# Kernel optimization log

Measured on AMD Instinct MI355X. Metric: run time of the kernel, lower is better.

The kernel has to match this reference:

```python
import jax, jax.numpy as jnp
import numpy as np

E = 1024   # embed_dim
H = 8      # att_heads
HD = E // H
L = 4      # layer_num
B = 64
M = 256
EPS = 1e-5


def celu(x, alpha=1.3):
    return jnp.where(x > 0, x, alpha * jnp.expm1(x / alpha))


def group_norm(x, w, b):
    # x: [N, E], groups = H (GroupNorm over channel groups, per-sample)
    xg = x.reshape(-1, H, HD)
    mu = xg.mean(-1, keepdims=True)
    var = ((xg - mu) ** 2).mean(-1, keepdims=True)
    xg = (xg - mu) * jax.lax.rsqrt(var + EPS)
    return xg.reshape(-1, E) * w + b


def layer_norm(x, w, b):
    mu = x.mean(-1, keepdims=True)
    var = ((x - mu) ** 2).mean(-1, keepdims=True)
    return (x - mu) * jax.lax.rsqrt(var + EPS) * w + b


def setup_inputs() -> dict:
    key = jax.random.key(0)
    ks = jax.random.split(key, 20)
    s = 0.02
    return {
        "gv_feat": jnp.zeros((B, 1), jnp.float32),
        "att_feats": jax.random.normal(ks[0], (B, M, E), jnp.float32),
        "att_mask": jnp.ones((B, M), jnp.float32),
        "mem_W": jax.random.normal(ks[1], (L, E, E), jnp.float32) * s,
        "mem_b": jnp.zeros((L, E), jnp.float32),
        "gn_w": jnp.ones((L, E), jnp.float32),
        "gn_b": jnp.zeros((L, E), jnp.float32),
        "upd_W": jax.random.normal(ks[2], (L, 2 * HD, HD), jnp.float32) * s,
        "upd_b": jnp.zeros((L, HD), jnp.float32),
        "gate_W": jax.random.normal(ks[3], (L, 2 * HD, HD), jnp.float32) * s,
        "gate_b": jnp.zeros((L, HD), jnp.float32),
        "ln_w": jnp.ones((L, E), jnp.float32),
        "ln_b": jnp.zeros((L, E), jnp.float32),
        "proj_W": jax.random.normal(ks[4], ((L + 1) * E, E), jnp.float32) * s,
        "proj_b": jnp.zeros((E,), jnp.float32),
        "lnf_w": jnp.ones((E,), jnp.float32),
        "lnf_b": jnp.zeros((E,), jnp.float32),
    }


def reference(gv_feat, att_feats, att_mask, mem_W, mem_b, gn_w, gn_b,
              upd_W, upd_b, gate_W, gate_b, ln_w, ln_b,
              proj_W, proj_b, lnf_w, lnf_b):
    scaling = HD ** (-0.5)
    mask3 = att_mask[:, :, None]                       # [B, M, 1]
    msum = mask3.sum(1)                                # [B, 1]

    def pool(x):
        return (x * mask3).sum(1) / msum               # [B, E]

    # gv_feat has last dim 1 -> computed by masked mean pooling
    gv = pool(att_feats)
    feat_arr = [gv]
    x = att_feats
    key_mask = att_mask[:, None, None, :]              # [B, 1, 1, M]
    for i in range(L):
        mem = celu(x.reshape(-1, E) @ mem_W[i] + mem_b[i])
        mem = group_norm(mem, gn_w[i], gn_b[i])
        xh = x.reshape(B, M, H, HD).swapaxes(1, 2)     # [B, H, M, HD]
        mh = mem.reshape(B, M, H, HD).swapaxes(1, 2)   # [B, H, M, HD]
        attn = jnp.einsum('bhqd,bhkd->bhqk', xh, mh) * scaling
        attn = jnp.where(key_mask == 0, -1e9, attn)
        p = jax.nn.softmax(attn, axis=-1)
        ctx = jnp.einsum('bhqk,bhkd->bhqd', p, xh)     # values == xh
        inp = jnp.concatenate([xh, ctx], axis=-1)      # [B, H, M, 2*HD]
        f_t = jnp.tanh(jax.nn.relu(inp @ upd_W[i] + upd_b[i]))  # dropout = eval identity
        g_t = jax.nn.sigmoid(inp @ gate_W[i] + gate_b[i])
        xh = g_t * f_t + (1.0 - g_t) * xh
        x = xh.swapaxes(1, 2).reshape(B, M, E)
        x = layer_norm(x, ln_w[i], ln_b[i])
        feat_arr.append(pool(x))
    gv = jnp.concatenate(feat_arr, axis=-1) @ proj_W + proj_b
    gv = layer_norm(gv, lnf_w, lnf_b)
    return gv, x
```

## Files before the change

### kernel.cpp

```cpp
#include <hip/hip_runtime.h>
#include <hip/hip_bf16.h>
#include <cstdint>
#include <cstddef>

typedef __bf16 v8bf __attribute__((ext_vector_type(8)));
typedef __bf16 v4bf __attribute__((ext_vector_type(4)));
typedef float  f32x4 __attribute__((ext_vector_type(4)));

typedef __attribute__((address_space(1))) void gas_void;
typedef __attribute__((address_space(3))) void las_void;

__device__ __forceinline__ void gload_lds16(const void* g, void* l) {
  __builtin_amdgcn_global_load_lds((const gas_void*)g, (las_void*)l, 16, 0, 0);
}

__device__ __forceinline__ float rdv(const void* p, size_t idx, int isf) {
  return isf ? ((const float*)p)[idx] : (float)((const __bf16*)p)[idx];
}

#define PB 64
#define PM 256
#define PE 1024
#define PH 8
#define PHD 128

__global__ void detect_kernel(const void* mask, int* flags) {
  if (threadIdx.x == 0) {
    uint32_t w = *(const uint32_t*)mask;
    flags[0] = ((w >> 16) == 0x3F80u && (w & 0xFFFFu) == 0x3F80u) ? 0 : 1;
  }
}

__global__ __launch_bounds__(256) void convx_kernel(
    const void* __restrict__ src, const int* __restrict__ flags, __bf16* __restrict__ dst) {
  const size_t i = ((size_t)blockIdx.x * 256 + threadIdx.x) * 4;
  if (flags[0]) {
    const float* s = (const float*)src + i;
    v4bf o; o[0] = (__bf16)s[0]; o[1] = (__bf16)s[1]; o[2] = (__bf16)s[2]; o[3] = (__bf16)s[3];
    *(v4bf*)(dst + i) = o;
  } else {
    *(v4bf*)(dst + i) = *(const v4bf*)((const __bf16*)src + i);
  }
}

__global__ __launch_bounds__(256) void transpose_kernel(
    const void* __restrict__ src, size_t soff, size_t zsrc, const int* __restrict__ flags,
    __bf16* __restrict__ dst, size_t zdst, int K, int N) {
  __shared__ __bf16 tile[64][66];
  const int isf = flags[0];
  const size_t so = soff + (size_t)blockIdx.z * zsrc;
  __bf16* d = dst + (size_t)blockIdx.z * zdst;
  const int n0 = blockIdx.x * 64, k0 = blockIdx.y * 64;
  const int c = threadIdx.x & 63, r0 = threadIdx.x >> 6;
#pragma unroll
  for (int j = 0; j < 16; ++j) {
    const int r = j * 4 + r0;
    tile[r][c] = (__bf16)rdv(src, so + (size_t)(k0 + r) * N + (n0 + c), isf);
  }
  __syncthreads();
#pragma unroll
  for (int j = 0; j < 16; ++j) {
    const int r = j * 4 + r0;
    d[(size_t)(n0 + r) * K + k0 + c] = tile[c][r];
  }
}

__global__ __launch_bounds__(256) void ugtr_kernel(
    const void* __restrict__ updW, const void* __restrict__ gateW,
    const int* __restrict__ flags, __bf16* __restrict__ ugWt) {
  __shared__ __bf16 tile[64][66];
  const int isf = flags[0];
  const int z = blockIdx.z, i = z >> 1, g = z & 1;
  const void* src = g ? gateW : updW;
  const size_t soff = (size_t)i * 32768;
  __bf16* dst = ugWt + (size_t)i * 65536 + g * 32768;
  const int n0 = blockIdx.x * 64, k0 = blockIdx.y * 64;
  const int c = threadIdx.x & 63, r0 = threadIdx.x >> 6;
#pragma unroll
  for (int j = 0; j < 16; ++j) {
    const int r = j * 4 + r0;
    tile[r][c] = (__bf16)rdv(src, soff + (size_t)(k0 + r) * 128 + (n0 + c), isf);
  }
  __syncthreads();
#pragma unroll
  for (int j = 0; j < 16; ++j) {
    const int r = j * 4 + r0;
    dst[(size_t)(n0 + r) * 256 + k0 + c] = tile[c][r];
  }
}

template<int AMODE, int BMODE, int ACT, bool OUTF32, bool CLAMPM, bool GNF, bool SPLITK, bool SWZ>
__global__ __launch_bounds__(256) void gemm_kernel(
    const __bf16* __restrict__ A, const __bf16* __restrict__ A2,
    const __bf16* __restrict__ Bt,
    const void* __restrict__ bias_a, int offa, const void* __restrict__ bias_b, int offb,
    int bias_split, const int* __restrict__ flags,
    const void* __restrict__ gnw, const void* __restrict__ gnb, int gnoff,
    void* __restrict__ Cout, int K, int Kfull, int Ntot, int Mtot)
{
  __shared__ __align__(16) uint8_t a_s[2][16384];
  __shared__ __align__(16) uint8_t b_s[2][16384];
  __shared__ float gnsum[128][2];
  __shared__ float gnsq[128][2];
  int bx = blockIdx.x, by = blockIdx.y;
  if (SWZ) {
    const int nx = gridDim.x;
    const int flat = by * nx + bx;
    const int xcd = flat & 7, slot = flat >> 3;
    by = slot & 7;
    bx = (slot >> 3) * 8 + xcd;
  }
  const int mbase = bx * 128;
  const int nbase = by * 128;
  const int koff = SPLITK ? blockIdx.z * K : 0;
  const int tid = threadIdx.x;
  const int wid = tid >> 6, lane = tid & 63;
  const int wr = wid >> 1, wc = wid & 1;

  f32x4 acc[4][4];
#pragma unroll
  for (int m = 0; m < 4; ++m)
#pragma unroll
    for (int n = 0; n < 4; ++n) acc[m][n] = (f32x4){0.f, 0.f, 0.f, 0.f};

  const int nkt = K >> 6;
  const int lrow8 = lane >> 3;
  const int cc = (lane & 7) << 4;

  auto STAGE = [&](int kt, uint8_t* as, uint8_t* bs) {
    const int kbase = koff + (kt << 6);
#pragma unroll
    for (int j = 0; j < 4; ++j) {
      const int q = wid * 4 + j;
      const int row = q * 8 + lrow8;
      const int c = cc ^ ((row & 7) << 4);
      const int klocal = c >> 1;
      const __bf16* asrc;
      if (AMODE == 0) {
        int rg = mbase + row;
        if (CLAMPM && rg > Mtot - 1) rg = Mtot - 1;
        asrc = A + (size_t)rg * Kfull + (kbase + klocal);
      } else {
        const int rg = mbase + row;
        const int kg = kbase + klocal;
        if (kg < PHD) {
          const int bh = rg >> 8, mm = rg & 255;
          const int bb = bh >> 3, hh = bh & 7;
          asrc = A + ((size_t)(bb * PM + mm) * PE + hh * PHD + kg);
        } else {
          asrc = A2 + ((size_t)rg * PHD + (kg - PHD));
        }
      }
      gload_lds16(asrc, as + q * 1024);
      const __bf16* bsrc;
      if (BMODE == 0) {
        bsrc = Bt + (size_t)(nbase + row) * Kfull + (kbase + klocal);
      } else {
        bsrc = Bt + (size_t)(mbase >> 8) * (PHD * PM)
                  + (size_t)(nbase + row) * Kfull + (kbase + klocal);
      }
      gload_lds16(bsrc, bs + q * 1024);
    }
  };

  STAGE(0, a_s[0], b_s[0]);
  if (nkt > 1) STAGE(1, a_s[1], b_s[1]);

  for (int kt = 0; kt < nkt; ++kt) {
    if (kt + 1 < nkt) asm volatile("s_waitcnt vmcnt(8)" ::: "memory");
    else              asm volatile("s_waitcnt vmcnt(0)" ::: "memory");
    __builtin_amdgcn_s_barrier();
    __builtin_amdgcn_sched_barrier(0);
    const uint8_t* ap = a_s[kt & 1];
    const uint8_t* bp = b_s[kt & 1];
#pragma unroll
    for (int kk = 0; kk < 2; ++kk) {
      const int co = kk * 64 + ((lane >> 4) << 4);
      v8bf af[4], bfr[4];
#pragma unroll
      for (int m = 0; m < 4; ++m) {
        const int row = wr * 64 + m * 16 + (lane & 15);
        af[m] = *(const v8bf*)(ap + row * 128 + (co ^ ((row & 7) << 4)));
      }
#pragma unroll
      for (int n = 0; n < 4; ++n) {
        const int row = wc * 64 + n * 16 + (lane & 15);
        bfr[n] = *(const v8bf*)(bp + row * 128 + (co ^ ((row & 7) << 4)));
      }
#pragma unroll
      for (int m = 0; m < 4; ++m)
#pragma unroll
        for (int n = 0; n < 4; ++n)
          acc[m][n] = __builtin_amdgcn_mfma_f32_16x16x32_bf16(af[m], bfr[n], acc[m][n], 0, 0, 0);
    }
    __builtin_amdgcn_s_barrier();
    __builtin_amdgcn_sched_barrier(0);
    if (kt + 2 < nkt) STAGE(kt + 2, a_s[kt & 1], b_s[kt & 1]);
  }

  const int isf = flags[0];
  if constexpr (GNF) {
    float bv[4];
#pragma unroll
    for (int n = 0; n < 4; ++n) {
      const int col = nbase + wc * 64 + n * 16 + (lane & 15);
      bv[n] = (bias_a != nullptr) ? rdv(bias_a, offa + col, isf) : 0.f;
    }
#pragma unroll
    for (int m = 0; m < 4; ++m)
#pragma unroll
      for (int n = 0; n < 4; ++n)
#pragma unroll
        for (int r = 0; r < 4; ++r) {
          float v = acc[m][n][r] + bv[n];
          if (ACT == 1) v = (v > 0.f) ? v : 1.3f * expm1f(v * (1.0f / 1.3f));
          acc[m][n][r] = v;
        }
#pragma unroll
    for (int m = 0; m < 4; ++m)
#pragma unroll
      for (int r = 0; r < 4; ++r) {
        float s = 0.f, q = 0.f;
#pragma unroll
        for (int n = 0; n < 4; ++n) { s += acc[m][n][r]; q += acc[m][n][r] * acc[m][n][r]; }
#pragma unroll
        for (int off = 1; off < 16; off <<= 1) {
          s += __shfl_xor(s, off, 64); q += __shfl_xor(q, off, 64);
        }
        const int lrow = wr * 64 + m * 16 + ((lane >> 4) << 2) + r;
        if ((lane & 15) == 0) { gnsum[lrow][wc] = s; gnsq[lrow][wc] = q; }
      }
    __syncthreads();
#pragma unroll
    for (int m = 0; m < 4; ++m)
#pragma unroll
      for (int r = 0; r < 4; ++r) {
        const int lrow = wr * 64 + m * 16 + ((lane >> 4) << 2) + r;
        const float mean = (gnsum[lrow][0] + gnsum[lrow][1]) * (1.f / 128.f);
        const float var = (gnsq[lrow][0] + gnsq[lrow][1]) * (1.f / 128.f) - mean * mean;
        const float rstd = rsqrtf(var + 1e-5f);
        const int rg = mbase + lrow;
#pragma unroll
        for (int n = 0; n < 4; ++n) {
          const int col = nbase + wc * 64 + n * 16 + (lane & 15);
          const float o = (acc[m][n][r] - mean) * rstd * rdv(gnw, gnoff + col, isf)
                          + rdv(gnb, gnoff + col, isf);
          ((__bf16*)Cout)[(size_t)rg * Ntot + col] = (__bf16)o;
        }
      }
  } else {
    float* coutF = (float*)Cout + (SPLITK ? (size_t)blockIdx.z * 65536 : (size_t)0);
#pragma unroll
    for (int m = 0; m < 4; ++m) {
      const int rowt = mbase + wr * 64 + m * 16 + ((lane >> 4) << 2);
#pragma unroll
      for (int n = 0; n < 4; ++n) {
        const int col = nbase + wc * 64 + n * 16 + (lane & 15);
        float bvv = 0.f;
        if (bias_a != nullptr)
          bvv = (col < bias_split) ? rdv(bias_a, offa + col, isf)
                                   : rdv(bias_b, offb + col - bias_split, isf);
#pragma unroll
        for (int r = 0; r < 4; ++r) {
          const int rg = rowt + r;
          if (CLAMPM && rg >= Mtot) continue;
          float v = acc[m][n][r] + bvv;
          if (ACT == 1) v = (v > 0.f) ? v : 1.3f * expm1f(v * (1.0f / 1.3f));
          if (OUTF32) coutF[(size_t)rg * Ntot + col] = v;
          else        ((__bf16*)Cout)[(size_t)rg * Ntot + col] = (__bf16)v;
        }
      }
    }
  }
}

__global__ __launch_bounds__(256) void attn_softmax_kernel(
    const __bf16* __restrict__ xc, const __bf16* __restrict__ memc,
    const void* __restrict__ mask, const int* __restrict__ flags, int b0,
    __bf16* __restrict__ S)
{
  const int bhl = blockIdx.x;
  const int bl = bhl >> 3, h = bhl & 7;
  const int isf = flags[0];
  const int tid = threadIdx.x, wid = tid >> 6, lane = tid & 63;
  const int qbase = blockIdx.y * 64 + wid * 16;
  const size_t xoff = (size_t)bl * PM * PE + h * PHD;

  v8bf a[4];
  {
    const int row = qbase + (lane & 15);
    const int d0 = (lane >> 4) * 8;
    const __bf16* p = xc + xoff + (size_t)row * PE + d0;
#pragma unroll
    for (int k = 0; k < 4; ++k) a[k] = *(const v8bf*)(p + k * 32);
  }
  float mz[16];
#pragma unroll
  for (int t = 0; t < 16; ++t)
    mz[t] = rdv(mask, (size_t)(b0 + bl) * PM + t * 16 + (lane & 15), isf);

  f32x4 acc[16];
#pragma unroll
  for (int t = 0; t < 16; ++t) acc[t] = (f32x4){0.f, 0.f, 0.f, 0.f};
#pragma unroll
  for (int t = 0; t < 16; ++t) {
    const int key = t * 16 + (lane & 15);
    const int d0 = (lane >> 4) * 8;
    const __bf16* p = memc + xoff + (size_t)key * PE + d0;
#pragma unroll
    for (int k = 0; k < 4; ++k) {
      v8bf bb = *(const v8bf*)(p + k * 32);
      acc[t] = __builtin_amdgcn_mfma_f32_16x16x32_bf16(a[k], bb, acc[t], 0, 0, 0);
    }
  }
  const float scale = 0.08838834764831845f;
  float mx[4], sm[4];
#pragma unroll
  for (int r = 0; r < 4; ++r) mx[r] = -3.0e38f;
#pragma unroll
  for (int t = 0; t < 16; ++t)
#pragma unroll
    for (int r = 0; r < 4; ++r) {
      float v = (mz[t] == 0.f) ? -1.0e9f : acc[t][r] * scale;
      acc[t][r] = v;
      mx[r] = fmaxf(mx[r], v);
    }
#pragma unroll
  for (int off = 1; off < 16; off <<= 1)
#pragma unroll
    for (int r = 0; r < 4; ++r) mx[r] = fmaxf(mx[r], __shfl_xor(mx[r], off, 64));
#pragma unroll
  for (int r = 0; r < 4; ++r) sm[r] = 0.f;
#pragma unroll
  for (int t = 0; t < 16; ++t)
#pragma unroll
    for (int r = 0; r < 4; ++r) {
      float e = expf(acc[t][r] - mx[r]);
      acc[t][r] = e; sm[r] += e;
    }
#pragma unroll
  for (int off = 1; off < 16; off <<= 1)
#pragma unroll
    for (int r = 0; r < 4; ++r) sm[r] += __shfl_xor(sm[r], off, 64);
#pragma unroll
  for (int r = 0; r < 4; ++r) sm[r] = 1.f / sm[r];

  const size_t srow = (size_t)bhl * PM;
#pragma unroll
  for (int r = 0; r < 4; ++r) {
    const int q = qbase + (lane >> 4) * 4 + r;
    __bf16* sp = S + (srow + q) * PM;
#pragma unroll
    for (int t = 0; t < 16; ++t)
      sp[t * 16 + (lane & 15)] = (__bf16)(acc[t][r] * sm[r]);
  }
}

__global__ __launch_bounds__(256) void transpose_x_kernel(
    const __bf16* __restrict__ xc, __bf16* __restrict__ xT)
{
  const int bh = blockIdx.x;
  const int b = bh >> 3, h = bh & 7;
  const int tz = blockIdx.y;
  const int d0 = (tz & 1) * 64, m0 = (tz >> 1) * 64;
  __shared__ __bf16 tile[64][66];
  const int c = threadIdx.x & 63, r0 = threadIdx.x >> 6;
  const __bf16* src = xc + ((size_t)b * PM + m0) * PE + h * PHD + d0;
#pragma unroll
  for (int j = 0; j < 16; ++j) {
    const int r = j * 4 + r0;
    tile[r][c] = src[(size_t)r * PE + c];
  }
  __syncthreads();
  __bf16* dst = xT + ((size_t)bh * PHD + d0) * PM + m0;
#pragma unroll
  for (int j = 0; j < 16; ++j) {
    const int r = j * 4 + r0;
    dst[(size_t)r * PM + c] = tile[c][r];
  }
}

__global__ __launch_bounds__(256) void gatingln_kernel(
    const __bf16* __restrict__ ug, const __bf16* __restrict__ xc,
    const void* __restrict__ w, const void* __restrict__ bz, int off,
    const int* __restrict__ flags, __bf16* __restrict__ xout,
    void* __restrict__ outAux, int row0)
{
  const size_t row = blockIdx.x;
  const int tid = threadIdx.x, wid = tid >> 6, lane = tid & 63;
  const int isf = flags[0];
  const int e = tid * 4, h = tid >> 5, d = e & 127;
  const size_t b = row >> 8; const int m = (int)(row & 255);
  const size_t ugrow = ((b * PH + h) * PM + m);
  v4bf fv = *(const v4bf*)(ug + ugrow * 256 + d);
  v4bf gvv = *(const v4bf*)(ug + ugrow * 256 + 128 + d);
  v4bf xv = *(const v4bf*)(xc + row * PE + e);
  float o[4];
#pragma unroll
  for (int r = 0; r < 4; ++r) {
    float f = fv[r], g = gvv[r], xh = xv[r];
    float gs = 1.f / (1.f + expf(-g));
    float ft = tanhf(fmaxf(f, 0.f));
    o[r] = gs * ft + (1.f - gs) * xh;
  }
  float s = o[0] + o[1] + o[2] + o[3];
  float q = o[0] * o[0] + o[1] * o[1] + o[2] * o[2] + o[3] * o[3];
#pragma unroll
  for (int off2 = 1; off2 < 64; off2 <<= 1) {
    s += __shfl_xor(s, off2, 64); q += __shfl_xor(q, off2, 64);
  }
  __shared__ float ss[4], qq[4];
  if (lane == 0) { ss[wid] = s; qq[wid] = q; }
  __syncthreads();
  s = ss[0] + ss[1] + ss[2] + ss[3];
  q = qq[0] + qq[1] + qq[2] + qq[3];
  const float mean = s * (1.f / 1024.f);
  const float var = q * (1.f / 1024.f) - mean * mean;
  const float rstd = rsqrtf(var + 1e-5f);
  float ov[4];
#pragma unroll
  for (int r = 0; r < 4; ++r)
    ov[r] = (o[r] - mean) * rstd * rdv(w, off + e + r, isf) + rdv(bz, off + e + r, isf);
  v4bf vo; vo[0] = (__bf16)ov[0]; vo[1] = (__bf16)ov[1]; vo[2] = (__bf16)ov[2]; vo[3] = (__bf16)ov[3];
  *(v4bf*)(xout + row * PE + e) = vo;
  if (outAux != nullptr) {
    const size_t idx = 65536 + (size_t)(row0 + row) * PE + e;
    if (isf) {
      float* op = (float*)outAux;
      op[idx] = ov[0]; op[idx + 1] = ov[1]; op[idx + 2] = ov[2]; op[idx + 3] = ov[3];
    } else {
      __bf16* op = (__bf16*)outAux;
      op[idx] = (__bf16)ov[0]; op[idx + 1] = (__bf16)ov[1];
      op[idx + 2] = (__bf16)ov[2]; op[idx + 3] = (__bf16)ov[3];
    }
  }
}

__global__ void msum_kernel(const void* __restrict__ mask, const int* __restrict__ flags,
                            float* __restrict__ msum)
{
  const int b = blockIdx.x, t = threadIdx.x;
  const int isf = flags[0];
  float s = 0.f;
#pragma unroll
  for (int j = 0; j < 4; ++j) s += rdv(mask, (size_t)b * PM + j * 64 + t, isf);
#pragma unroll
  for (int off = 1; off < 64; off <<= 1) s += __shfl_xor(s, off, 64);
  if (t == 0) msum[b] = s;
}

__global__ __launch_bounds__(1024) void pool_kernel(
    const __bf16* __restrict__ x, const void* __restrict__ mask, const int* __restrict__ flags,
    const float* __restrict__ msum, __bf16* __restrict__ feats, int colOff)
{
  __shared__ float red[4][256];
  const int b = blockIdx.x;
  const int el = threadIdx.x & 255;
  const int wq = threadIdx.x >> 8;
  const int e = blockIdx.y * 256 + el;
  const int isf = flags[0];
  const __bf16* p = x + (size_t)b * PM * PE + e;
  float acc = 0.f;
  const int m0 = wq * 64;
  for (int m = m0; m < m0 + 64; m += 4) {
#pragma unroll
    for (int j = 0; j < 4; ++j)
      acc += (float)p[(size_t)(m + j) * PE] * rdv(mask, (size_t)b * PM + m + j, isf);
  }
  red[wq][el] = acc;
  __syncthreads();
  if (wq == 0) {
    float s = red[0][el] + red[1][el] + red[2][el] + red[3][el];
    feats[(size_t)b * (5 * PE) + colOff + e] = (__bf16)(s / msum[b]);
  }
}

__global__ __launch_bounds__(256) void projreduce_kernel(
    const float* __restrict__ part, const void* __restrict__ pb,
    const int* __restrict__ flags, float* __restrict__ gvpre)
{
  const int row = blockIdx.x;
  const int c0 = threadIdx.x * 4;
  const int isf = flags[0];
  float a0 = rdv(pb, c0 + 0, isf), a1 = rdv(pb, c0 + 1, isf);
  float a2 = rdv(pb, c0 + 2, isf), a3 = rdv(pb, c0 + 3, isf);
#pragma unroll
  for (int z = 0; z < 8; ++z) {
    const float* p = part + (size_t)z * 65536 + (size_t)row * 1024 + c0;
    a0 += p[0]; a1 += p[1]; a2 += p[2]; a3 += p[3];
  }
  float* op = gvpre + (size_t)row * 1024 + c0;
  op[0] = a0; op[1] = a1; op[2] = a2; op[3] = a3;
}

__global__ __launch_bounds__(256) void ln_final_kernel(
    const float* __restrict__ gin, const void* __restrict__ w, const void* __restrict__ bz,
    const int* __restrict__ flags, void* __restrict__ out)
{
  const size_t row = blockIdx.x;
  const int tid = threadIdx.x, wid = tid >> 6, lane = tid & 63;
  const int isf = flags[0];
  const float* p = gin + row * PE + tid * 4;
  float f0 = p[0], f1 = p[1], f2 = p[2], f3 = p[3];
  float s = f0 + f1 + f2 + f3;
  float q = f0 * f0 + f1 * f1 + f2 * f2 + f3 * f3;
#pragma unroll
  for (int off = 1; off < 64; off <<= 1) {
    s += __shfl_xor(s, off, 64); q += __shfl_xor(q, off, 64);
  }
  __shared__ float ss[4], qq[4];
  if (lane == 0) { ss[wid] = s; qq[wid] = q; }
  __syncthreads();
  s = ss[0] + ss[1] + ss[2] + ss[3];
  q = qq[0] + qq[1] + qq[2] + qq[3];
  const float mean = s * (1.f / 1024.f);
  const float var = q * (1.f / 1024.f) - mean * mean;
  const float rstd = rsqrtf(var + 1e-5f);
  const int e = tid * 4;
#pragma unroll
  for (int j = 0; j < 4; ++j) {
    const float fj = (j == 0 ? f0 : j == 1 ? f1 : j == 2 ? f2 : f3);
    const float ov = (fj - mean) * rstd * rdv(w, e + j, isf) + rdv(bz, e + j, isf);
    if (isf) ((float*)out)[row * PE + e + j] = ov;
    else     ((__bf16*)out)[row * PE + e + j] = (__bf16)ov;
  }
}

extern "C" void kernel_launch(void* const* d_in, const int* in_sizes, int n_in,
                              void* d_out, int out_size, void* d_ws, size_t ws_size,
                              hipStream_t stream) {
  const void* att_feats = d_in[1];
  const void* att_mask  = d_in[2];
  const void* mem_W  = d_in[3];
  const void* mem_b  = d_in[4];
  const void* gn_w   = d_in[5];
  const void* gn_b   = d_in[6];
  const void* upd_W  = d_in[7];
  const void* upd_b  = d_in[8];
  const void* gate_W = d_in[9];
  const void* gate_b = d_in[10];
  const void* ln_w   = d_in[11];
  const void* ln_b   = d_in[12];
  const void* proj_W = d_in[13];
  const void* proj_b = d_in[14];
  const void* lnf_w  = d_in[15];
  const void* lnf_b  = d_in[16];

  uint8_t* ws = (uint8_t*)d_ws;
  int*    flags  = (int*)ws;
  float*  msum   = (float*)(ws + 4096);
  __bf16* featsb = (__bf16*)(ws + 8192);
  float*  gvpre  = (float*)(ws + 665600);
  __bf16* memWt  = (__bf16*)(ws + 1048576);
  __bf16* ugWt   = (__bf16*)(ws + 9437184);
  __bf16* xa0    = (__bf16*)(ws + 10485760);
  __bf16* xa     = (__bf16*)(ws + 44040192);
  uint8_t* dynb  = ws + 77594624;

  int NC;
  if (ws_size >= (size_t)211812352) NC = 1;
  else if (ws_size >= (size_t)144703488) NC = 2;
  else NC = 4;
  const int CSd = PB / NC;
  const int CROWSd = CSd * PM;
  const int CGRd = CSd * PH * PM;
  const size_t CB = (size_t)CROWSd * PE * 2;
  __bf16* membc = (__bf16*)dynb;
  __bf16* xTgc  = (__bf16*)(dynb + CB);
  __bf16* sbufc = (__bf16*)(dynb + 2 * CB);

  detect_kernel<<<1, 64, 0, stream>>>(att_mask, flags);
  convx_kernel<<<16384, 256, 0, stream>>>(att_feats, flags, xa0);

  transpose_kernel<<<dim3(16, 16, 4), 256, 0, stream>>>(
      mem_W, 0, 1048576, flags, memWt, 1048576, 1024, 1024);
  ugtr_kernel<<<dim3(2, 4, 8), 256, 0, stream>>>(upd_W, gate_W, flags, ugWt);

  msum_kernel<<<64, 64, 0, stream>>>(att_mask, flags, msum);
  pool_kernel<<<dim3(64, 4), 1024, 0, stream>>>(xa0, att_mask, flags, msum, featsb, 0);

  const __bf16* xcur = xa0;
  for (int i = 0; i < 4; ++i) {
    for (int c = 0; c < NC; ++c) {
      const __bf16* xc = xcur + (size_t)c * CROWSd * PE;
      gemm_kernel<0, 0, 1, false, false, true, false, true><<<dim3(CROWSd / 128, 8), 256, 0, stream>>>(
          xc, nullptr, memWt + (size_t)i * 1048576, mem_b, i * 1024, nullptr, 0, 1024,
          flags, gn_w, gn_b, i * 1024, membc, 1024, 1024, 1024, CROWSd);
      transpose_x_kernel<<<dim3(CSd * 8, 8), 256, 0, stream>>>(xc, xTgc);
      attn_softmax_kernel<<<dim3(CSd * 8, 4), 256, 0, stream>>>(xc, membc, att_mask, flags,
                                                                c * CSd, sbufc);
      gemm_kernel<0, 1, 0, false, false, false, false, false><<<dim3(CGRd / 128, 1), 256, 0, stream>>>(
          sbufc, nullptr, xTgc, nullptr, 0, nullptr, 0, 128, flags, nullptr, nullptr, 0,
          membc, 256, 256, 128, CGRd);
      gemm_kernel<1, 0, 0, false, false, false, false, false><<<dim3(CGRd / 128, 2), 256, 0, stream>>>(
          xc, membc, ugWt + (size_t)i * 65536, upd_b, i * 128, gate_b, i * 128, 128,
          flags, nullptr, nullptr, 0, sbufc, 256, 256, 256, CGRd);
      gatingln_kernel<<<CROWSd, 256, 0, stream>>>(sbufc, xc, ln_w, ln_b, i * 1024, flags,
                                                  xa + (size_t)c * CROWSd * PE,
                                                  (i == 3) ? d_out : nullptr, c * CROWSd);
    }
    pool_kernel<<<dim3(64, 4), 1024, 0, stream>>>(xa, att_mask, flags, msum, featsb,
                                                  (i + 1) * 1024);
    xcur = xa;
  }

  __bf16* projWt = sbufc;
  float* projPart = (float*)dynb;
  transpose_kernel<<<dim3(16, 80, 1), 256, 0, stream>>>(proj_W, 0, 0, flags, projWt, 0, 5120, 1024);
  gemm_kernel<0, 0, 0, true, true, false, true, false><<<dim3(1, 8, 8), 256, 0, stream>>>(
      featsb, nullptr, projWt, nullptr, 0, nullptr, 0, 1024,
      flags, nullptr, nullptr, 0, projPart, 640, 5120, 1024, 64);
  projreduce_kernel<<<64, 256, 0, stream>>>(projPart, proj_b, flags, gvpre);
  ln_final_kernel<<<64, 256, 0, stream>>>(gvpre, lnf_w, lnf_b, flags, d_out);
}
```

Measured before the change: 1.427 ms.

## Load GEMM B operand directly into registers instead of staging through LDS

The B tile is no longer copied into shared memory. Each wave now reads its B fragments straight from global memory into registers, one k-tile ahead, while A keeps its double-buffered LDS staging and the vmcnt waits are retuned to match. This halves LDS use and removes the B LDS reads, which could allow higher occupancy. In exchange, the two column waves in each row load the same B data redundantly, the global loads are less coalesced (16-byte chunks per lane spread across rows), and register pressure goes up.

```diff
diff --git a/kernel.cpp b/kernel.cpp
--- a/kernel.cpp
+++ b/kernel.cpp
@@ -99,7 +99,6 @@
     void* __restrict__ Cout, int K, int Kfull, int Ntot, int Mtot)
 {
   __shared__ __align__(16) uint8_t a_s[2][16384];
-  __shared__ __align__(16) uint8_t b_s[2][16384];
   __shared__ float gnsum[128][2];
   __shared__ float gnsq[128][2];
   int bx = blockIdx.x, by = blockIdx.y;
@@ -127,7 +126,14 @@
   const int lrow8 = lane >> 3;
   const int cc = (lane & 7) << 4;
 
-  auto STAGE = [&](int kt, uint8_t* as, uint8_t* bs) {
+  const __bf16* bpan = Bt + (BMODE == 1 ? (size_t)(mbase >> 8) * (PHD * PM) : (size_t)0);
+  size_t browOff[4];
+#pragma unroll
+  for (int n = 0; n < 4; ++n)
+    browOff[n] = (size_t)(nbase + wc * 64 + n * 16 + (lane & 15)) * Kfull;
+  const int bk_lane = (lane >> 4) << 3;
+
+  auto STAGE_A = [&](int kt, uint8_t* as) {
     const int kbase = koff + (kt << 6);
 #pragma unroll
     for (int j = 0; j < 4; ++j) {
@@ -152,50 +158,51 @@
         }
       }
       gload_lds16(asrc, as + q * 1024);
-      const __bf16* bsrc;
-      if (BMODE == 0) {
-        bsrc = Bt + (size_t)(nbase + row) * Kfull + (kbase + klocal);
-      } else {
-        bsrc = Bt + (size_t)(mbase >> 8) * (PHD * PM)
-                  + (size_t)(nbase + row) * Kfull + (kbase + klocal);
-      }
-      gload_lds16(bsrc, bs + q * 1024);
     }
   };
 
-  STAGE(0, a_s[0], b_s[0]);
-  if (nkt > 1) STAGE(1, a_s[1], b_s[1]);
+  v8bf bfr[2][4];
+  auto LOADB = [&](int kt) {
+    const int kb = koff + (kt << 6);
+#pragma unroll
+    for (int kk = 0; kk < 2; ++kk)
+#pragma unroll
+      for (int n = 0; n < 4; ++n)
+        bfr[kk][n] = *(const v8bf*)(bpan + browOff[n] + kb + kk * 32 + bk_lane);
+  };
+
+  STAGE_A(0, a_s[0]);
+  __builtin_amdgcn_sched_barrier(0);
+  LOADB(0);
+  __builtin_amdgcn_sched_barrier(0);
+  if (nkt > 1) STAGE_A(1, a_s[1]);
 
   for (int kt = 0; kt < nkt; ++kt) {
-    if (kt + 1 < nkt) asm volatile("s_waitcnt vmcnt(8)" ::: "memory");
-    else              asm volatile("s_waitcnt vmcnt(0)" ::: "memory");
+    if (kt + 1 < nkt) asm volatile("s_waitcnt vmcnt(12)" ::: "memory");
+    else              asm volatile("s_waitcnt vmcnt(8)" ::: "memory");
     __builtin_amdgcn_s_barrier();
     __builtin_amdgcn_sched_barrier(0);
     const uint8_t* ap = a_s[kt & 1];
-    const uint8_t* bp = b_s[kt & 1];
 #pragma unroll
     for (int kk = 0; kk < 2; ++kk) {
       const int co = kk * 64 + ((lane >> 4) << 4);
-      v8bf af[4], bfr[4];
+      v8bf af[4];
 #pragma unroll
       for (int m = 0; m < 4; ++m) {
         const int row = wr * 64 + m * 16 + (lane & 15);
         af[m] = *(const v8bf*)(ap + row * 128 + (co ^ ((row & 7) << 4)));
       }
 #pragma unroll
-      for (int n = 0; n < 4; ++n) {
-        const int row = wc * 64 + n * 16 + (lane & 15);
-        bfr[n] = *(const v8bf*)(bp + row * 128 + (co ^ ((row & 7) << 4)));
-      }
-#pragma unroll
       for (int m = 0; m < 4; ++m)
 #pragma unroll
         for (int n = 0; n < 4; ++n)
-          acc[m][n] = __builtin_amdgcn_mfma_f32_16x16x32_bf16(af[m], bfr[n], acc[m][n], 0, 0, 0);
+          acc[m][n] = __builtin_amdgcn_mfma_f32_16x16x32_bf16(af[m], bfr[kk][n], acc[m][n], 0, 0, 0);
     }
     __builtin_amdgcn_s_barrier();
     __builtin_amdgcn_sched_barrier(0);
-    if (kt + 2 < nkt) STAGE(kt + 2, a_s[kt & 1], b_s[kt & 1]);
+    if (kt + 1 < nkt) LOADB(kt + 1);
+    __builtin_amdgcn_sched_barrier(0);
+    if (kt + 2 < nkt) STAGE_A(kt + 2, a_s[kt & 1]);
   }
 
   const int isf = flags[0];
```

Result: slower. 1.566 ms (+9.7%).

## Stage GEMM tiles through registers instead of direct global-to-LDS loads

Applied to the files above, without the earlier changes.

The GEMM main loop stops using global_load_lds to fill shared memory. Each thread now loads its 16-byte slices of the next A/B tile into registers with ordinary vector loads and writes them, swizzled, into the alternate LDS buffer at the top of the following iteration. This gives the compiler normal load dependencies to schedule, so the explicit vmcnt waits before the barrier go away. In exchange it costs extra VGPRs for the staging registers and extra ds_write instructions, which may lower occupancy.

```diff
diff --git a/kernel.cpp b/kernel.cpp
--- a/kernel.cpp
+++ b/kernel.cpp
@@ -6,13 +6,7 @@
 typedef __bf16 v8bf __attribute__((ext_vector_type(8)));
 typedef __bf16 v4bf __attribute__((ext_vector_type(4)));
 typedef float  f32x4 __attribute__((ext_vector_type(4)));
-
-typedef __attribute__((address_space(1))) void gas_void;
-typedef __attribute__((address_space(3))) void las_void;
-
-__device__ __forceinline__ void gload_lds16(const void* g, void* l) {
-  __builtin_amdgcn_global_load_lds((const gas_void*)g, (las_void*)l, 16, 0, 0);
-}
+typedef uint32_t v4u __attribute__((ext_vector_type(4)));
 
 __device__ __forceinline__ float rdv(const void* p, size_t idx, int isf) {
   return isf ? ((const float*)p)[idx] : (float)((const __bf16*)p)[idx];
@@ -125,51 +119,64 @@
 
   const int nkt = K >> 6;
   const int lrow8 = lane >> 3;
-  const int cc = (lane & 7) << 4;
-
-  auto STAGE = [&](int kt, uint8_t* as, uint8_t* bs) {
-    const int kbase = koff + (kt << 6);
+  const int klin = (lane & 7) << 3;
+
+  v4u Ar[4], Br[4];
+
+  auto LOADT = [&](int kt) {
+    const int kbase = koff + (kt << 6) + klin;
 #pragma unroll
     for (int j = 0; j < 4; ++j) {
       const int q = wid * 4 + j;
       const int row = q * 8 + lrow8;
-      const int c = cc ^ ((row & 7) << 4);
-      const int klocal = c >> 1;
       const __bf16* asrc;
       if (AMODE == 0) {
         int rg = mbase + row;
         if (CLAMPM && rg > Mtot - 1) rg = Mtot - 1;
-        asrc = A + (size_t)rg * Kfull + (kbase + klocal);
+        asrc = A + (size_t)rg * Kfull + kbase;
       } else {
         const int rg = mbase + row;
-        const int kg = kbase + klocal;
-        if (kg < PHD) {
+        if (kbase < PHD) {
           const int bh = rg >> 8, mm = rg & 255;
           const int bb = bh >> 3, hh = bh & 7;
-          asrc = A + ((size_t)(bb * PM + mm) * PE + hh * PHD + kg);
+          asrc = A + ((size_t)(bb * PM + mm) * PE + hh * PHD + kbase);
         } else {
-          asrc = A2 + ((size_t)rg * PHD + (kg - PHD));
+          asrc = A2 + ((size_t)rg * PHD + (kbase - PHD));
         }
       }
-      gload_lds16(asrc, as + q * 1024);
+      Ar[j] = *(const v4u*)asrc;
       const __bf16* bsrc;
       if (BMODE == 0) {
-        bsrc = Bt + (size_t)(nbase + row) * Kfull + (kbase + klocal);
+        bsrc = Bt + (size_t)(nbase + row) * Kfull + kbase;
       } else {
         bsrc = Bt + (size_t)(mbase >> 8) * (PHD * PM)
-                  + (size_t)(nbase + row) * Kfull + (kbase + klocal);
+                  + (size_t)(nbase + row) * Kfull + kbase;
       }
-      gload_lds16(bsrc, bs + q * 1024);
+      Br[j] = *(const v4u*)bsrc;
     }
   };
 
-  STAGE(0, a_s[0], b_s[0]);
-  if (nkt > 1) STAGE(1, a_s[1], b_s[1]);
+  auto WRITET = [&](int buf) {
+#pragma unroll
+    for (int j = 0; j < 4; ++j) {
+      const int q = wid * 4 + j;
+      const int row = q * 8 + lrow8;
+      const int dst = row * 128 + (((lane & 7) << 4) ^ ((row & 7) << 4));
+      *(v4u*)(a_s[buf] + dst) = Ar[j];
+      *(v4u*)(b_s[buf] + dst) = Br[j];
+    }
+  };
+
+  LOADT(0);
+  WRITET(0);
+  if (nkt > 1) LOADT(1);
+  asm volatile("s_waitcnt lgkmcnt(0)" ::: "memory");
+  __builtin_amdgcn_s_barrier();
+  __builtin_amdgcn_sched_barrier(0);
 
   for (int kt = 0; kt < nkt; ++kt) {
-    if (kt + 1 < nkt) asm volatile("s_waitcnt vmcnt(8)" ::: "memory");
-    else              asm volatile("s_waitcnt vmcnt(0)" ::: "memory");
-    __builtin_amdgcn_s_barrier();
+    if (kt + 1 < nkt) WRITET((kt + 1) & 1);
+    if (kt + 2 < nkt) LOADT(kt + 2);
     __builtin_amdgcn_sched_barrier(0);
     const uint8_t* ap = a_s[kt & 1];
     const uint8_t* bp = b_s[kt & 1];
@@ -193,9 +200,9 @@
         for (int n = 0; n < 4; ++n)
           acc[m][n] = __builtin_amdgcn_mfma_f32_16x16x32_bf16(af[m], bfr[n], acc[m][n], 0, 0, 0);
     }
+    asm volatile("s_waitcnt lgkmcnt(0)" ::: "memory");
     __builtin_amdgcn_s_barrier();
     __builtin_amdgcn_sched_barrier(0);
-    if (kt + 2 < nkt) STAGE(kt + 2, a_s[kt & 1], b_s[kt & 1]);
   }
 
   const int isf = flags[0];
```

Result: faster. 1.379 ms (-3.4%).
